# Kernel tuning notes

Measured on AMD Instinct MI355X. Metric: run time of the kernel, lower is better.

Reference implementation:

```python
import jax, jax.numpy as jnp
import numpy as np

NO, NR, E, D = 50000, 2000, 600000, 128
NEG_SLOPE = 0.2


def setup_inputs() -> dict:
    key = jax.random.key(0)
    ks = jax.random.split(key, 16)
    p = lambda k, shape: jax.random.normal(k, shape, dtype=jnp.float32) * 0.05
    return {
        "x_order": jax.random.normal(ks[0], (NO, D), dtype=jnp.float32),
        "x_rider": jax.random.normal(ks[1], (NR, D), dtype=jnp.float32),
        "order_idx": jax.random.randint(ks[2], (E,), 0, NO),
        "rider_idx": jax.random.randint(ks[3], (E,), 0, NR),
        # GATConv layer 1 (order_input_dim=128 -> hidden_dim=128, heads=1)
        "Ws1": p(ks[4], (D, D)), "Wd1": p(ks[5], (D, D)),
        "as1": p(ks[6], (D,)), "ad1": p(ks[7], (D,)), "b1": jnp.zeros((D,), jnp.float32),
        # GATConv layer 2 (hidden_dim=128 -> output_dim=128, heads=1)
        "Ws2": p(ks[8], (D, D)), "Wd2": p(ks[9], (D, D)),
        "as2": p(ks[10], (D,)), "ad2": p(ks[11], (D,)), "b2": jnp.zeros((D,), jnp.float32),
    }


def _segment_softmax(e, seg, num_segments):
    # numerically-stable softmax over edges grouped by destination node
    m = jax.ops.segment_max(e, seg, num_segments=num_segments)
    ex = jnp.exp(e - m[seg])
    s = jax.ops.segment_sum(ex, seg, num_segments=num_segments)
    return ex / (s[seg] + 1e-16)


def _gat_bipartite(x_src, x_dst, oi, ri, Ws, Wd, a_src, a_dst, b, n_dst):
    # PyG GATConv, heads=1, bipartite (src=order, dst=rider), no self-loops
    hs = x_src @ Ws            # [NO, D]
    hd = x_dst @ Wd            # [NR, D]
    alpha_s = hs @ a_src       # [NO]
    alpha_d = hd @ a_dst       # [NR]
    e = jax.nn.leaky_relu(alpha_s[oi] + alpha_d[ri], NEG_SLOPE)  # [E]
    alpha = _segment_softmax(e, ri, n_dst)                        # [E]
    out = jax.ops.segment_sum(alpha[:, None] * hs[oi], ri, num_segments=n_dst)
    return out + b


def reference(x_order, x_rider, order_idx, rider_idx,
              Ws1, Wd1, as1, ad1, b1, Ws2, Wd2, as2, ad2, b2):
    n_rider = x_rider.shape[0]
    # layer 1: update riders; order features pass through
    r1 = jax.nn.relu(_gat_bipartite(x_order, x_rider, order_idx, rider_idx,
                                    Ws1, Wd1, as1, ad1, b1, n_rider))
    o1 = jax.nn.relu(x_order)
    # layer 2
    r2 = _gat_bipartite(o1, r1, order_idx, rider_idx,
                        Ws2, Wd2, as2, ad2, b2, n_rider)
    # per-edge gather-dot-sigmoid scoring
    scores = jnp.sum(o1[order_idx] * r2[rider_idx], axis=1)
    return jax.nn.sigmoid(scores)
```

## Files before the change

### kernel.cpp

```cpp
#include <hip/hip_runtime.h>
#include <hip/hip_fp16.h>
#include <math.h>

#define NO 50000
#define NR 2000
#define NE 600000
#define D  128
#define NEG_SLOPE 0.2f
#define CAP 448
#define SLOT 512
#define NB 256
#define CH ((NE + NB - 1) / NB)

__global__ void precompute_wv(const float* __restrict__ Ws1, const float* __restrict__ as1,
                              const float* __restrict__ Wd1, const float* __restrict__ ad1,
                              const float* __restrict__ Ws2, const float* __restrict__ as2,
                              const float* __restrict__ Wd2, const float* __restrict__ ad2,
                              float* __restrict__ wsv1, float* __restrict__ wdv1,
                              float* __restrict__ wsv2, float* __restrict__ wdv2) {
    int k = threadIdx.x;
    float s1 = 0.f, d1 = 0.f, s2 = 0.f, d2 = 0.f;
    for (int j = 0; j < D; ++j) {
        s1 += Ws1[k * D + j] * as1[j];
        d1 += Wd1[k * D + j] * ad1[j];
        s2 += Ws2[k * D + j] * as2[j];
        d2 += Wd2[k * D + j] * ad2[j];
    }
    wsv1[k] = s1; wdv1[k] = d1; wsv2[k] = s2; wdv2[k] = d2;
}

__global__ void node_prep(const float* __restrict__ x, const float* __restrict__ xr,
                          const float* __restrict__ wsv1, const float* __restrict__ wsv2,
                          const float* __restrict__ wdv1,
                          float* __restrict__ as1o, float* __restrict__ as2o,
                          float* __restrict__ ad1r, __half* __restrict__ x16) {
    int lane = threadIdx.x & 63;
    if (blockIdx.x < NO / 4) {
        int row = blockIdx.x * 4 + (threadIdx.x >> 6);
        float2 xv = ((const float2*)(x + (size_t)row * D))[lane];
        float2 w1 = ((const float2*)wsv1)[lane];
        float2 w2 = ((const float2*)wsv2)[lane];
        float rx0 = fmaxf(xv.x, 0.f), rx1 = fmaxf(xv.y, 0.f);
        ((__half2*)(x16 + (size_t)row * D))[lane] = __floats2half2_rn(xv.x, xv.y);
        float a1 = xv.x * w1.x + xv.y * w1.y;
        float a2 = rx0 * w2.x + rx1 * w2.y;
        for (int off = 32; off; off >>= 1) {
            a1 += __shfl_down(a1, off);
            a2 += __shfl_down(a2, off);
        }
        if (lane == 0) { as1o[row] = a1; as2o[row] = a2; }
    } else {
        int row = (blockIdx.x - NO / 4) * 4 + (threadIdx.x >> 6);
        float2 xv = ((const float2*)(xr + (size_t)row * D))[lane];
        float2 w1 = ((const float2*)wdv1)[lane];
        float a = xv.x * w1.x + xv.y * w1.y;
        for (int off = 32; off; off >>= 1) a += __shfl_down(a, off);
        if (lane == 0) ad1r[row] = a;
    }
}


__global__ void blockhist_kernel(const int* __restrict__ ri, int* __restrict__ blockHist) {
    __shared__ int h[NR];
    int b = blockIdx.x, t = threadIdx.x;
    for (int i = t; i < NR; i += 256) h[i] = 0;
    __syncthreads();
    int lo = b * CH;
    int hi = lo + CH; if (hi > NE) hi = NE;
    for (int i = lo + t; i < hi; i += 256) atomicAdd(&h[ri[i]], 1);
    __syncthreads();
    for (int i = t; i < NR; i += 256) blockHist[(size_t)b * NR + i] = h[i];
}

__global__ void rowscan_kernel(int* __restrict__ blockHist, int* __restrict__ total) {
    int lane = threadIdx.x & 63;
    int r = blockIdx.x * 4 + (threadIdx.x >> 6);
    if (r >= NR) return;
    int b0 = lane * 4;
    int v0 = blockHist[(size_t)(b0 + 0) * NR + r];
    int v1 = blockHist[(size_t)(b0 + 1) * NR + r];
    int v2 = blockHist[(size_t)(b0 + 2) * NR + r];
    int v3 = blockHist[(size_t)(b0 + 3) * NR + r];
    int s = v0 + v1 + v2 + v3;
    int incl = s;
    for (int off = 1; off < 64; off <<= 1) {
        int u = __shfl_up(incl, off);
        if (lane >= off) incl += u;
    }
    int base = incl - s;
    blockHist[(size_t)(b0 + 0) * NR + r] = base;
    blockHist[(size_t)(b0 + 1) * NR + r] = base + v0;
    blockHist[(size_t)(b0 + 2) * NR + r] = base + v0 + v1;
    blockHist[(size_t)(b0 + 3) * NR + r] = base + v0 + v1 + v2;
    int tot = __shfl(incl, 63);
    if (lane == 0) total[r] = tot;
}

__global__ void scatter_kernel(const int* __restrict__ oi, const int* __restrict__ ri,
                               const int* __restrict__ blockHist,
                               int* __restrict__ sOrd, int* __restrict__ sEid) {
    __shared__ int h[NR];
    int b = blockIdx.x, t = threadIdx.x;
    for (int i = t; i < NR; i += 256) h[i] = 0;
    __syncthreads();
    int lo = b * CH;
    int hi = lo + CH; if (hi > NE) hi = NE;
    for (int i = lo + t; i < hi; i += 256) {
        int r = ri[i];
        int rank = atomicAdd(&h[r], 1);
        int pos = r * SLOT + blockHist[(size_t)b * NR + r] + rank;
        sOrd[pos] = oi[i];
        sEid[pos] = i;
    }
}

__global__ void __launch_bounds__(256)
rider_fused(const __half* __restrict__ x16,
            const float* __restrict__ as1o, const float* __restrict__ as2o,
            const float* __restrict__ ad1r,
            const int* __restrict__ cnt,
            const int* __restrict__ sOrd, const int* __restrict__ sEid,
            const float* __restrict__ W1, const float* __restrict__ b1,
            const float* __restrict__ wdv2,
            const float* __restrict__ W2, const float* __restrict__ b2,
            float* __restrict__ out) {
    __shared__ float eL[CAP];
    __shared__ float a2L[CAP];
    __shared__ int   sO[CAP];
    __shared__ int   sE[CAP];
    __shared__ float red[256];
    __shared__ float red8[256][9];
    __shared__ float tl[D];
    __shared__ float r2L[D];
    int r = blockIdx.x, t = threadIdx.x;
    int base = r * SLOT, n = cnt[r];
    float ad1 = ad1r[r];
    int grp = t >> 4, lh = t & 15;

    float s1 = 0.f;
    for (int i = t; i < n; i += 256) {
        int o = sOrd[base + i];
        float a2v = as2o[o];
        float e = as1o[o] + ad1;
        e = (e > 0.f) ? e : NEG_SLOPE * e;
        float ex = __expf(e);
        if (i < CAP) { eL[i] = ex; a2L[i] = a2v; sO[i] = o; sE[i] = sEid[base + i]; }
        s1 += ex;
    }
    red[t] = s1;
    __syncthreads();
    for (int off = 128; off; off >>= 1) {
        if (t < off) red[t] += red[t + off];
        __syncthreads();
    }
    float inv1 = 1.f / (red[0] + 1e-16f);
    __syncthreads();

    {
        float acc[8];
#pragma unroll
        for (int k = 0; k < 8; ++k) acc[k] = 0.f;
        if (n <= CAP) {
            int i = grp;
            for (; i + 16 < n; i += 32) {
                float a0 = eL[i], a1 = eL[i + 16];
                uint4 h0 = ((const uint4*)(x16 + (size_t)sO[i] * D))[lh];
                uint4 h1 = ((const uint4*)(x16 + (size_t)sO[i + 16] * D))[lh];
                const __half2* p0 = (const __half2*)&h0;
                const __half2* p1 = (const __half2*)&h1;
#pragma unroll
                for (int q = 0; q < 4; ++q) {
                    float2 f0 = __half22float2(p0[q]);
                    float2 f1 = __half22float2(p1[q]);
                    acc[2 * q]     += a0 * f0.x + a1 * f1.x;
                    acc[2 * q + 1] += a0 * f0.y + a1 * f1.y;
                }
            }
            if (i < n) {
                float a0 = eL[i];
                uint4 h0 = ((const uint4*)(x16 + (size_t)sO[i] * D))[lh];
                const __half2* p0 = (const __half2*)&h0;
#pragma unroll
                for (int q = 0; q < 4; ++q) {
                    float2 f0 = __half22float2(p0[q]);
                    acc[2 * q]     += a0 * f0.x;
                    acc[2 * q + 1] += a0 * f0.y;
                }
            }
        } else {
            for (int i = grp; i < n; i += 16) {
                float a0; int o;
                if (i < CAP) { a0 = eL[i]; o = sO[i]; }
                else {
                    o = sOrd[base + i];
                    float e = as1o[o] + ad1;
                    e = (e > 0.f) ? e : NEG_SLOPE * e;
                    a0 = __expf(e);
                }
                uint4 h0 = ((const uint4*)(x16 + (size_t)o * D))[lh];
                const __half2* p0 = (const __half2*)&h0;
#pragma unroll
                for (int q = 0; q < 4; ++q) {
                    float2 f0 = __half22float2(p0[q]);
                    acc[2 * q]     += a0 * f0.x;
                    acc[2 * q + 1] += a0 * f0.y;
                }
            }
        }
#pragma unroll
        for (int k = 0; k < 8; ++k) red8[t][k] = acc[k];
    }
    __syncthreads();
    if (t < D) {
        int lh2 = t >> 3, k = t & 7;
        float s = 0.f;
        for (int g = 0; g < 16; ++g) s += red8[g * 16 + lh2][k];
        tl[t] = s * inv1;
    }
    __syncthreads();

    {
        int d = t & 127, h = t >> 7;
        float a = 0.f;
        for (int k = h * 64; k < h * 64 + 64; ++k) a += tl[k] * W1[k * D + d];
        red[t] = a;
        __syncthreads();
        if (t < 128) red[t] = fmaxf(red[t] + red[t + 128] + b1[t], 0.f) * wdv2[t];
        __syncthreads();
        for (int off = 64; off; off >>= 1) {
            if (t < off) red[t] += red[t + off];
            __syncthreads();
        }
    }
    float ad2 = red[0];
    __syncthreads();

    float s2 = 0.f;
    for (int i = t; i < n; i += 256) {
        float a2v = (i < CAP) ? a2L[i] : as2o[sOrd[base + i]];
        float e = a2v + ad2;
        e = (e > 0.f) ? e : NEG_SLOPE * e;
        float ex = __expf(e);
        if (i < CAP) eL[i] = ex;
        s2 += ex;
    }
    red[t] = s2;
    __syncthreads();
    for (int off = 128; off; off >>= 1) {
        if (t < off) red[t] += red[t + off];
        __syncthreads();
    }
    float inv2 = 1.f / (red[0] + 1e-16f);
    __syncthreads();

    {
        float acc[8];
#pragma unroll
        for (int k = 0; k < 8; ++k) acc[k] = 0.f;
        if (n <= CAP) {
            int i = grp;
            for (; i + 16 < n; i += 32) {
                float a0 = eL[i], a1 = eL[i + 16];
                uint4 h0 = ((const uint4*)(x16 + (size_t)sO[i] * D))[lh];
                uint4 h1 = ((const uint4*)(x16 + (size_t)sO[i + 16] * D))[lh];
                const __half2* p0 = (const __half2*)&h0;
                const __half2* p1 = (const __half2*)&h1;
#pragma unroll
                for (int q = 0; q < 4; ++q) {
                    float2 f0 = __half22float2(p0[q]);
                    float2 f1 = __half22float2(p1[q]);
                    acc[2 * q]     += a0 * fmaxf(f0.x, 0.f) + a1 * fmaxf(f1.x, 0.f);
                    acc[2 * q + 1] += a0 * fmaxf(f0.y, 0.f) + a1 * fmaxf(f1.y, 0.f);
                }
            }
            if (i < n) {
                float a0 = eL[i];
                uint4 h0 = ((const uint4*)(x16 + (size_t)sO[i] * D))[lh];
                const __half2* p0 = (const __half2*)&h0;
#pragma unroll
                for (int q = 0; q < 4; ++q) {
                    float2 f0 = __half22float2(p0[q]);
                    acc[2 * q]     += a0 * fmaxf(f0.x, 0.f);
                    acc[2 * q + 1] += a0 * fmaxf(f0.y, 0.f);
                }
            }
        } else {
            for (int i = grp; i < n; i += 16) {
                float a0; int o;
                if (i < CAP) { a0 = eL[i]; o = sO[i]; }
                else {
                    o = sOrd[base + i];
                    float e = as2o[o] + ad2;
                    e = (e > 0.f) ? e : NEG_SLOPE * e;
                    a0 = __expf(e);
                }
                uint4 h0 = ((const uint4*)(x16 + (size_t)o * D))[lh];
                const __half2* p0 = (const __half2*)&h0;
#pragma unroll
                for (int q = 0; q < 4; ++q) {
                    float2 f0 = __half22float2(p0[q]);
                    acc[2 * q]     += a0 * fmaxf(f0.x, 0.f);
                    acc[2 * q + 1] += a0 * fmaxf(f0.y, 0.f);
                }
            }
        }
#pragma unroll
        for (int k = 0; k < 8; ++k) red8[t][k] = acc[k];
    }
    __syncthreads();
    if (t < D) {
        int lh2 = t >> 3, k = t & 7;
        float s = 0.f;
        for (int g = 0; g < 16; ++g) s += red8[g * 16 + lh2][k];
        tl[t] = s * inv2;
    }
    __syncthreads();

    {
        int d = t & 127, h = t >> 7;
        float a = 0.f;
        for (int k = h * 64; k < h * 64 + 64; ++k) a += tl[k] * W2[k * D + d];
        red[t] = a;
        __syncthreads();
        if (t < 128) r2L[t] = red[t] + red[t + 128] + b2[t];
        __syncthreads();
    }

    float rv[8];
#pragma unroll
    for (int k = 0; k < 8; ++k) rv[k] = r2L[lh * 8 + k];
    for (int i = grp; i < n; i += 16) {
        int o, eid;
        if (i < CAP) { o = sO[i]; eid = sE[i]; }
        else { o = sOrd[base + i]; eid = sEid[base + i]; }
        uint4 h0 = ((const uint4*)(x16 + (size_t)o * D))[lh];
        const __half2* p0 = (const __half2*)&h0;
        float p = 0.f;
#pragma unroll
        for (int q = 0; q < 4; ++q) {
            float2 f0 = __half22float2(p0[q]);
            p += fmaxf(f0.x, 0.f) * rv[2 * q] + fmaxf(f0.y, 0.f) * rv[2 * q + 1];
        }
        p += __shfl_xor(p, 8);
        p += __shfl_xor(p, 4);
        p += __shfl_xor(p, 2);
        p += __shfl_xor(p, 1);
        if (lh == 0) out[eid] = 1.f / (1.f + __expf(-p));
    }
}

extern "C" void kernel_launch(void* const* d_in, const int* in_sizes, int n_in,
                              void* d_out, int out_size, void* d_ws, size_t ws_size,
                              hipStream_t stream) {
    const float* x_order = (const float*)d_in[0];
    const float* x_rider = (const float*)d_in[1];
    const int*   oi      = (const int*)d_in[2];
    const int*   ri      = (const int*)d_in[3];
    const float* Ws1 = (const float*)d_in[4];
    const float* Wd1 = (const float*)d_in[5];
    const float* as1 = (const float*)d_in[6];
    const float* ad1 = (const float*)d_in[7];
    const float* b1  = (const float*)d_in[8];
    const float* Ws2 = (const float*)d_in[9];
    const float* Wd2 = (const float*)d_in[10];
    const float* as2 = (const float*)d_in[11];
    const float* ad2 = (const float*)d_in[12];
    const float* b2  = (const float*)d_in[13];
    float* out = (float*)d_out;

    char* w = (char*)d_ws;
    float* wsv1 = (float*)w; w += 512;
    float* wdv1 = (float*)w; w += 512;
    float* wsv2 = (float*)w; w += 512;
    float* wdv2 = (float*)w; w += 512;
    float* as1o = (float*)w; w += (size_t)NO * 4;
    float* as2o = (float*)w; w += (size_t)NO * 4;
    float* ad1r = (float*)w; w += (size_t)NR * 4;
    int* total  = (int*)w;   w += (size_t)NR * 4;
    int* blockHist = (int*)w; w += (size_t)NB * NR * 4;
    int* sOrd   = (int*)w;   w += (size_t)NR * SLOT * 4;
    int* sEid   = (int*)w;   w += (size_t)NR * SLOT * 4;
    __half* x16 = (__half*)w; w += (size_t)NO * D * 2;

    precompute_wv<<<1, 128, 0, stream>>>(Ws1, as1, Wd1, ad1, Ws2, as2, Wd2, ad2,
                                         wsv1, wdv1, wsv2, wdv2);
    node_prep<<<NO / 4 + NR / 4, 256, 0, stream>>>(x_order, x_rider, wsv1, wsv2, wdv1,
                                                   as1o, as2o, ad1r, x16);

    blockhist_kernel<<<NB, 256, 0, stream>>>(ri, blockHist);
    rowscan_kernel<<<NR / 4, 256, 0, stream>>>(blockHist, total);
    scatter_kernel<<<NB, 256, 0, stream>>>(oi, ri, blockHist, sOrd, sEid);

    rider_fused<<<NR, 256, 0, stream>>>(x16, as1o, as2o, ad1r, total, sOrd, sEid,
                                        Ws1, b1, wdv2, Ws2, b2, out);
}
```

Before: 246.9 us.

## Split fused rider kernel into layer-1 aggregation and layer-2 aggregate-score kernels

Splits the single per-rider fused kernel into two launches. The first does the layer-1 softmax aggregation and projection and writes the per-rider layer-2 attention scalar to a new workspace buffer. The second recomputes the neighbour list and exponentials, then does the layer-2 aggregation and edge scoring. Each kernel uses less shared memory and fewer registers, which may raise occupancy, and the layer-1 gather loop is unrolled four-wide for more loads in flight. The cost is an extra launch plus re-reading sOrd and the as2 values in the second kernel.

```diff
diff --git a/kernel.cpp b/kernel.cpp
--- a/kernel.cpp
+++ b/kernel.cpp
@@ -115,17 +115,142 @@
 }
 
 __global__ void __launch_bounds__(256)
-rider_fused(const __half* __restrict__ x16,
-            const float* __restrict__ as1o, const float* __restrict__ as2o,
-            const float* __restrict__ ad1r,
-            const int* __restrict__ cnt,
-            const int* __restrict__ sOrd, const int* __restrict__ sEid,
-            const float* __restrict__ W1, const float* __restrict__ b1,
-            const float* __restrict__ wdv2,
-            const float* __restrict__ W2, const float* __restrict__ b2,
-            float* __restrict__ out) {
+rider_agg1(const __half* __restrict__ x16, const float* __restrict__ as_o,
+           const float* __restrict__ ad_r,
+           const int* __restrict__ cnt, const int* __restrict__ sOrd,
+           const float* __restrict__ W, const float* __restrict__ bias,
+           const float* __restrict__ wdv2, float* __restrict__ ad2r) {
     __shared__ float eL[CAP];
-    __shared__ float a2L[CAP];
+    __shared__ int   sO[CAP];
+    __shared__ float red[256];
+    __shared__ float red8[256][9];
+    __shared__ float tl[D];
+    int r = blockIdx.x, t = threadIdx.x;
+    int base = r * SLOT, n = cnt[r];
+    float ad = ad_r[r];
+    int grp = t >> 4, lh = t & 15;
+
+    float ls = 0.f;
+    for (int i = t; i < n; i += 256) {
+        int o = sOrd[base + i];
+        float e = as_o[o] + ad;
+        e = (e > 0.f) ? e : NEG_SLOPE * e;
+        float ex = __expf(e);
+        if (i < CAP) { eL[i] = ex; sO[i] = o; }
+        ls += ex;
+    }
+    red[t] = ls;
+    __syncthreads();
+    for (int off = 128; off; off >>= 1) {
+        if (t < off) red[t] += red[t + off];
+        __syncthreads();
+    }
+    float inv = 1.f / (red[0] + 1e-16f);
+    __syncthreads();
+
+    float acc[8];
+#pragma unroll
+    for (int k = 0; k < 8; ++k) acc[k] = 0.f;
+    if (n <= CAP) {
+        int i = grp;
+        for (; i + 48 < n; i += 64) {
+            float a0 = eL[i], a1 = eL[i + 16], a2 = eL[i + 32], a3 = eL[i + 48];
+            uint4 h0 = ((const uint4*)(x16 + (size_t)sO[i]      * D))[lh];
+            uint4 h1 = ((const uint4*)(x16 + (size_t)sO[i + 16] * D))[lh];
+            uint4 h2 = ((const uint4*)(x16 + (size_t)sO[i + 32] * D))[lh];
+            uint4 h3 = ((const uint4*)(x16 + (size_t)sO[i + 48] * D))[lh];
+            const __half2* p0 = (const __half2*)&h0;
+            const __half2* p1 = (const __half2*)&h1;
+            const __half2* p2 = (const __half2*)&h2;
+            const __half2* p3 = (const __half2*)&h3;
+#pragma unroll
+            for (int q = 0; q < 4; ++q) {
+                float2 f0 = __half22float2(p0[q]);
+                float2 f1 = __half22float2(p1[q]);
+                float2 f2 = __half22float2(p2[q]);
+                float2 f3 = __half22float2(p3[q]);
+                acc[2 * q]     += a0 * f0.x + a1 * f1.x + a2 * f2.x + a3 * f3.x;
+                acc[2 * q + 1] += a0 * f0.y + a1 * f1.y + a2 * f2.y + a3 * f3.y;
+            }
+        }
+        for (; i + 16 < n; i += 32) {
+            float a0 = eL[i], a1 = eL[i + 16];
+            uint4 h0 = ((const uint4*)(x16 + (size_t)sO[i]      * D))[lh];
+            uint4 h1 = ((const uint4*)(x16 + (size_t)sO[i + 16] * D))[lh];
+            const __half2* p0 = (const __half2*)&h0;
+            const __half2* p1 = (const __half2*)&h1;
+#pragma unroll
+            for (int q = 0; q < 4; ++q) {
+                float2 f0 = __half22float2(p0[q]);
+                float2 f1 = __half22float2(p1[q]);
+                acc[2 * q]     += a0 * f0.x + a1 * f1.x;
+                acc[2 * q + 1] += a0 * f0.y + a1 * f1.y;
+            }
+        }
+        if (i < n) {
+            float a0 = eL[i];
+            uint4 h0 = ((const uint4*)(x16 + (size_t)sO[i] * D))[lh];
+            const __half2* p0 = (const __half2*)&h0;
+#pragma unroll
+            for (int q = 0; q < 4; ++q) {
+                float2 f0 = __half22float2(p0[q]);
+                acc[2 * q]     += a0 * f0.x;
+                acc[2 * q + 1] += a0 * f0.y;
+            }
+        }
+    } else {
+        for (int i = grp; i < n; i += 16) {
+            float a0; int o;
+            if (i < CAP) { a0 = eL[i]; o = sO[i]; }
+            else {
+                o = sOrd[base + i];
+                float e = as_o[o] + ad;
+                e = (e > 0.f) ? e : NEG_SLOPE * e;
+                a0 = __expf(e);
+            }
+            uint4 h0 = ((const uint4*)(x16 + (size_t)o * D))[lh];
+            const __half2* p0 = (const __half2*)&h0;
+#pragma unroll
+            for (int q = 0; q < 4; ++q) {
+                float2 f0 = __half22float2(p0[q]);
+                acc[2 * q]     += a0 * f0.x;
+                acc[2 * q + 1] += a0 * f0.y;
+            }
+        }
+    }
+#pragma unroll
+    for (int k = 0; k < 8; ++k) red8[t][k] = acc[k];
+    __syncthreads();
+    if (t < D) {
+        int lh2 = t >> 3, k = t & 7;
+        float s = 0.f;
+        for (int g = 0; g < 16; ++g) s += red8[g * 16 + lh2][k];
+        tl[t] = s * inv;
+    }
+    __syncthreads();
+
+    int d = t & 127, h = t >> 7;
+    float a2 = 0.f;
+    for (int k = h * 64; k < h * 64 + 64; ++k) a2 += tl[k] * W[k * D + d];
+    red[t] = a2;
+    __syncthreads();
+    if (t < 128) red[t] = fmaxf(red[t] + red[t + 128] + bias[t], 0.f) * wdv2[t];
+    __syncthreads();
+    for (int off = 64; off; off >>= 1) {
+        if (t < off) red[t] += red[t + off];
+        __syncthreads();
+    }
+    if (t == 0) ad2r[r] = red[0];
+}
+
+__global__ void __launch_bounds__(256)
+agg2_score(const __half* __restrict__ x16, const float* __restrict__ as_o,
+           const float* __restrict__ ad_r,
+           const int* __restrict__ cnt,
+           const int* __restrict__ sOrd, const int* __restrict__ sEid,
+           const float* __restrict__ W, const float* __restrict__ bias,
+           float* __restrict__ out) {
+    __shared__ float eL[CAP];
     __shared__ int   sO[CAP];
     __shared__ int   sE[CAP];
     __shared__ float red[256];
@@ -134,195 +259,95 @@
     __shared__ float r2L[D];
     int r = blockIdx.x, t = threadIdx.x;
     int base = r * SLOT, n = cnt[r];
-    float ad1 = ad1r[r];
+    float ad = ad_r[r];
     int grp = t >> 4, lh = t & 15;
 
-    float s1 = 0.f;
+    float ls = 0.f;
     for (int i = t; i < n; i += 256) {
         int o = sOrd[base + i];
-        float a2v = as2o[o];
-        float e = as1o[o] + ad1;
+        float e = as_o[o] + ad;
         e = (e > 0.f) ? e : NEG_SLOPE * e;
         float ex = __expf(e);
-        if (i < CAP) { eL[i] = ex; a2L[i] = a2v; sO[i] = o; sE[i] = sEid[base + i]; }
-        s1 += ex;
-    }
-    red[t] = s1;
+        if (i < CAP) { eL[i] = ex; sO[i] = o; sE[i] = sEid[base + i]; }
+        ls += ex;
+    }
+    red[t] = ls;
     __syncthreads();
     for (int off = 128; off; off >>= 1) {
         if (t < off) red[t] += red[t + off];
         __syncthreads();
     }
-    float inv1 = 1.f / (red[0] + 1e-16f);
-    __syncthreads();
-
-    {
-        float acc[8];
-#pragma unroll
-        for (int k = 0; k < 8; ++k) acc[k] = 0.f;
-        if (n <= CAP) {
-            int i = grp;
-            for (; i + 16 < n; i += 32) {
-                float a0 = eL[i], a1 = eL[i + 16];
-                uint4 h0 = ((const uint4*)(x16 + (size_t)sO[i] * D))[lh];
-                uint4 h1 = ((const uint4*)(x16 + (size_t)sO[i + 16] * D))[lh];
-                const __half2* p0 = (const __half2*)&h0;
-                const __half2* p1 = (const __half2*)&h1;
-#pragma unroll
-                for (int q = 0; q < 4; ++q) {
-                    float2 f0 = __half22float2(p0[q]);
-                    float2 f1 = __half22float2(p1[q]);
-                    acc[2 * q]     += a0 * f0.x + a1 * f1.x;
-                    acc[2 * q + 1] += a0 * f0.y + a1 * f1.y;
-                }
-            }
-            if (i < n) {
-                float a0 = eL[i];
-                uint4 h0 = ((const uint4*)(x16 + (size_t)sO[i] * D))[lh];
-                const __half2* p0 = (const __half2*)&h0;
-#pragma unroll
-                for (int q = 0; q < 4; ++q) {
-                    float2 f0 = __half22float2(p0[q]);
-                    acc[2 * q]     += a0 * f0.x;
-                    acc[2 * q + 1] += a0 * f0.y;
-                }
-            }
-        } else {
-            for (int i = grp; i < n; i += 16) {
-                float a0; int o;
-                if (i < CAP) { a0 = eL[i]; o = sO[i]; }
-                else {
-                    o = sOrd[base + i];
-                    float e = as1o[o] + ad1;
-                    e = (e > 0.f) ? e : NEG_SLOPE * e;
-                    a0 = __expf(e);
-                }
-                uint4 h0 = ((const uint4*)(x16 + (size_t)o * D))[lh];
-                const __half2* p0 = (const __half2*)&h0;
-#pragma unroll
-                for (int q = 0; q < 4; ++q) {
-                    float2 f0 = __half22float2(p0[q]);
-                    acc[2 * q]     += a0 * f0.x;
-                    acc[2 * q + 1] += a0 * f0.y;
-                }
-            }
-        }
-#pragma unroll
-        for (int k = 0; k < 8; ++k) red8[t][k] = acc[k];
-    }
+    float inv = 1.f / (red[0] + 1e-16f);
+    __syncthreads();
+
+    float acc[8];
+#pragma unroll
+    for (int k = 0; k < 8; ++k) acc[k] = 0.f;
+    if (n <= CAP) {
+        int i = grp;
+        for (; i + 16 < n; i += 32) {
+            float a0 = eL[i], a1 = eL[i + 16];
+            uint4 h0 = ((const uint4*)(x16 + (size_t)sO[i]      * D))[lh];
+            uint4 h1 = ((const uint4*)(x16 + (size_t)sO[i + 16] * D))[lh];
+            const __half2* p0 = (const __half2*)&h0;
+            const __half2* p1 = (const __half2*)&h1;
+#pragma unroll
+            for (int q = 0; q < 4; ++q) {
+                float2 f0 = __half22float2(p0[q]);
+                float2 f1 = __half22float2(p1[q]);
+                acc[2 * q]     += a0 * fmaxf(f0.x, 0.f) + a1 * fmaxf(f1.x, 0.f);
+                acc[2 * q + 1] += a0 * fmaxf(f0.y, 0.f) + a1 * fmaxf(f1.y, 0.f);
+            }
+        }
+        if (i < n) {
+            float a0 = eL[i];
+            uint4 h0 = ((const uint4*)(x16 + (size_t)sO[i] * D))[lh];
+            const __half2* p0 = (const __half2*)&h0;
+#pragma unroll
+            for (int q = 0; q < 4; ++q) {
+                float2 f0 = __half22float2(p0[q]);
+                acc[2 * q]     += a0 * fmaxf(f0.x, 0.f);
+                acc[2 * q + 1] += a0 * fmaxf(f0.y, 0.f);
+            }
+        }
+    } else {
+        for (int i = grp; i < n; i += 16) {
+            float a0; int o;
+            if (i < CAP) { a0 = eL[i]; o = sO[i]; }
+            else {
+                o = sOrd[base + i];
+                float e = as_o[o] + ad;
+                e = (e > 0.f) ? e : NEG_SLOPE * e;
+                a0 = __expf(e);
+            }
+            uint4 h0 = ((const uint4*)(x16 + (size_t)o * D))[lh];
+            const __half2* p0 = (const __half2*)&h0;
+#pragma unroll
+            for (int q = 0; q < 4; ++q) {
+                float2 f0 = __half22float2(p0[q]);
+                acc[2 * q]     += a0 * fmaxf(f0.x, 0.f);
+                acc[2 * q + 1] += a0 * fmaxf(f0.y, 0.f);
+            }
+        }
+    }
+#pragma unroll
+    for (int k = 0; k < 8; ++k) red8[t][k] = acc[k];
     __syncthreads();
     if (t < D) {
         int lh2 = t >> 3, k = t & 7;
         float s = 0.f;
         for (int g = 0; g < 16; ++g) s += red8[g * 16 + lh2][k];
-        tl[t] = s * inv1;
+        tl[t] = s * inv;
     }
     __syncthreads();
 
     {
         int d = t & 127, h = t >> 7;
         float a = 0.f;
-        for (int k = h * 64; k < h * 64 + 64; ++k) a += tl[k] * W1[k * D + d];
+        for (int k = h * 64; k < h * 64 + 64; ++k) a += tl[k] * W[k * D + d];
         red[t] = a;
         __syncthreads();
-        if (t < 128) red[t] = fmaxf(red[t] + red[t + 128] + b1[t], 0.f) * wdv2[t];
-        __syncthreads();
-        for (int off = 64; off; off >>= 1) {
-            if (t < off) red[t] += red[t + off];
-            __syncthreads();
-        }
-    }
-    float ad2 = red[0];
-    __syncthreads();
-
-    float s2 = 0.f;
-    for (int i = t; i < n; i += 256) {
-        float a2v = (i < CAP) ? a2L[i] : as2o[sOrd[base + i]];
-        float e = a2v + ad2;
-        e = (e > 0.f) ? e : NEG_SLOPE * e;
-        float ex = __expf(e);
-        if (i < CAP) eL[i] = ex;
-        s2 += ex;
-    }
-    red[t] = s2;
-    __syncthreads();
-    for (int off = 128; off; off >>= 1) {
-        if (t < off) red[t] += red[t + off];
-        __syncthreads();
-    }
-    float inv2 = 1.f / (red[0] + 1e-16f);
-    __syncthreads();
-
-    {
-        float acc[8];
-#pragma unroll
-        for (int k = 0; k < 8; ++k) acc[k] = 0.f;
-        if (n <= CAP) {
-            int i = grp;
-            for (; i + 16 < n; i += 32) {
-                float a0 = eL[i], a1 = eL[i + 16];
-                uint4 h0 = ((const uint4*)(x16 + (size_t)sO[i] * D))[lh];
-                uint4 h1 = ((const uint4*)(x16 + (size_t)sO[i + 16] * D))[lh];
-                const __half2* p0 = (const __half2*)&h0;
-                const __half2* p1 = (const __half2*)&h1;
-#pragma unroll
-                for (int q = 0; q < 4; ++q) {
-                    float2 f0 = __half22float2(p0[q]);
-                    float2 f1 = __half22float2(p1[q]);
-                    acc[2 * q]     += a0 * fmaxf(f0.x, 0.f) + a1 * fmaxf(f1.x, 0.f);
-                    acc[2 * q + 1] += a0 * fmaxf(f0.y, 0.f) + a1 * fmaxf(f1.y, 0.f);
-                }
-            }
-            if (i < n) {
-                float a0 = eL[i];
-                uint4 h0 = ((const uint4*)(x16 + (size_t)sO[i] * D))[lh];
-                const __half2* p0 = (const __half2*)&h0;
-#pragma unroll
-                for (int q = 0; q < 4; ++q) {
-                    float2 f0 = __half22float2(p0[q]);
-                    acc[2 * q]     += a0 * fmaxf(f0.x, 0.f);
-                    acc[2 * q + 1] += a0 * fmaxf(f0.y, 0.f);
-                }
-            }
-        } else {
-            for (int i = grp; i < n; i += 16) {
-                float a0; int o;
-                if (i < CAP) { a0 = eL[i]; o = sO[i]; }
-                else {
-                    o = sOrd[base + i];
-                    float e = as2o[o] + ad2;
-                    e = (e > 0.f) ? e : NEG_SLOPE * e;
-                    a0 = __expf(e);
-                }
-                uint4 h0 = ((const uint4*)(x16 + (size_t)o * D))[lh];
-                const __half2* p0 = (const __half2*)&h0;
-#pragma unroll
-                for (int q = 0; q < 4; ++q) {
-                    float2 f0 = __half22float2(p0[q]);
-                    acc[2 * q]     += a0 * fmaxf(f0.x, 0.f);
-                    acc[2 * q + 1] += a0 * fmaxf(f0.y, 0.f);
-                }
-            }
-        }
-#pragma unroll
-        for (int k = 0; k < 8; ++k) red8[t][k] = acc[k];
-    }
-    __syncthreads();
-    if (t < D) {
-        int lh2 = t >> 3, k = t & 7;
-        float s = 0.f;
-        for (int g = 0; g < 16; ++g) s += red8[g * 16 + lh2][k];
-        tl[t] = s * inv2;
-    }
-    __syncthreads();
-
-    {
-        int d = t & 127, h = t >> 7;
-        float a = 0.f;
-        for (int k = h * 64; k < h * 64 + 64; ++k) a += tl[k] * W2[k * D + d];
-        red[t] = a;
-        __syncthreads();
-        if (t < 128) r2L[t] = red[t] + red[t + 128] + b2[t];
+        if (t < 128) r2L[t] = red[t] + red[t + 128] + bias[t];
         __syncthreads();
     }
 
@@ -376,6 +401,7 @@
     float* as1o = (float*)w; w += (size_t)NO * 4;
     float* as2o = (float*)w; w += (size_t)NO * 4;
     float* ad1r = (float*)w; w += (size_t)NR * 4;
+    float* ad2r = (float*)w; w += (size_t)NR * 4;
     int* total  = (int*)w;   w += (size_t)NR * 4;
     int* blockHist = (int*)w; w += (size_t)NB * NR * 4;
     int* sOrd   = (int*)w;   w += (size_t)NR * SLOT * 4;
@@ -391,6 +417,8 @@
     rowscan_kernel<<<NR / 4, 256, 0, stream>>>(blockHist, total);
     scatter_kernel<<<NB, 256, 0, stream>>>(oi, ri, blockHist, sOrd, sEid);
 
-    rider_fused<<<NR, 256, 0, stream>>>(x16, as1o, as2o, ad1r, total, sOrd, sEid,
-                                        Ws1, b1, wdv2, Ws2, b2, out);
-}
+    rider_agg1<<<NR, 256, 0, stream>>>(x16, as1o, ad1r, total, sOrd,
+                                       Ws1, b1, wdv2, ad2r);
+    agg2_score<<<NR, 256, 0, stream>>>(x16, as2o, ad2r, total, sOrd, sEid,
+                                       Ws2, b2, out);
+}
```

New measurement: 243.8 us. About the same (-1.3%).

## Merge prep kernels and move edge scoring into a separate edge-parallel kernel

Applied to the files above, without the earlier changes.

Merges the weight-vector precompute into the histogram kernel and the row scan into the node-prep kernel, cutting two launches. Edge scoring now runs in a new kernel parallel over edges in the original edge order, reading per-rider r2 stored as fp16, so the sEid scatter array and its writes go away. The work of each 2000-block rider kernel is shortened. The cost is an extra launch and a global round-trip for r2, plus reduced precision from storing r2 in fp16.

```diff
diff --git a/kernel.cpp b/kernel.cpp
--- a/kernel.cpp
+++ b/kernel.cpp
@@ -12,31 +12,47 @@
 #define NB 256
 #define CH ((NE + NB - 1) / NB)
 
-__global__ void precompute_wv(const float* __restrict__ Ws1, const float* __restrict__ as1,
-                              const float* __restrict__ Wd1, const float* __restrict__ ad1,
-                              const float* __restrict__ Ws2, const float* __restrict__ as2,
-                              const float* __restrict__ Wd2, const float* __restrict__ ad2,
-                              float* __restrict__ wsv1, float* __restrict__ wdv1,
-                              float* __restrict__ wsv2, float* __restrict__ wdv2) {
-    int k = threadIdx.x;
-    float s1 = 0.f, d1 = 0.f, s2 = 0.f, d2 = 0.f;
-    for (int j = 0; j < D; ++j) {
-        s1 += Ws1[k * D + j] * as1[j];
-        d1 += Wd1[k * D + j] * ad1[j];
-        s2 += Ws2[k * D + j] * as2[j];
-        d2 += Wd2[k * D + j] * ad2[j];
-    }
-    wsv1[k] = s1; wdv1[k] = d1; wsv2[k] = s2; wdv2[k] = d2;
-}
-
-__global__ void node_prep(const float* __restrict__ x, const float* __restrict__ xr,
+__global__ void prep_hist(const int* __restrict__ ri, int* __restrict__ blockHist,
+                          const float* __restrict__ Ws1, const float* __restrict__ as1,
+                          const float* __restrict__ Wd1, const float* __restrict__ ad1,
+                          const float* __restrict__ Ws2, const float* __restrict__ as2,
+                          const float* __restrict__ Wd2, const float* __restrict__ ad2,
+                          float* __restrict__ wsv1, float* __restrict__ wdv1,
+                          float* __restrict__ wsv2, float* __restrict__ wdv2) {
+    __shared__ int h[NR];
+    int t = threadIdx.x;
+    if (blockIdx.x < NB) {
+        int b = blockIdx.x;
+        for (int i = t; i < NR; i += 256) h[i] = 0;
+        __syncthreads();
+        int lo = b * CH;
+        int hi = lo + CH; if (hi > NE) hi = NE;
+        for (int i = lo + t; i < hi; i += 256) atomicAdd(&h[ri[i]], 1);
+        __syncthreads();
+        for (int i = t; i < NR; i += 256) blockHist[(size_t)b * NR + i] = h[i];
+    } else if (t < 128) {
+        int k = t;
+        float s1 = 0.f, d1 = 0.f, s2 = 0.f, d2 = 0.f;
+        for (int j = 0; j < D; ++j) {
+            s1 += Ws1[k * D + j] * as1[j];
+            d1 += Wd1[k * D + j] * ad1[j];
+            s2 += Ws2[k * D + j] * as2[j];
+            d2 += Wd2[k * D + j] * ad2[j];
+        }
+        wsv1[k] = s1; wdv1[k] = d1; wsv2[k] = s2; wdv2[k] = d2;
+    }
+}
+
+__global__ void prep_scan(const float* __restrict__ x, const float* __restrict__ xr,
                           const float* __restrict__ wsv1, const float* __restrict__ wsv2,
                           const float* __restrict__ wdv1,
                           float* __restrict__ as1o, float* __restrict__ as2o,
-                          float* __restrict__ ad1r, __half* __restrict__ x16) {
+                          float* __restrict__ ad1r, __half* __restrict__ x16,
+                          int* __restrict__ blockHist, int* __restrict__ total) {
     int lane = threadIdx.x & 63;
-    if (blockIdx.x < NO / 4) {
-        int row = blockIdx.x * 4 + (threadIdx.x >> 6);
+    int b = blockIdx.x;
+    if (b < NO / 4) {
+        int row = b * 4 + (threadIdx.x >> 6);
         float2 xv = ((const float2*)(x + (size_t)row * D))[lane];
         float2 w1 = ((const float2*)wsv1)[lane];
         float2 w2 = ((const float2*)wsv2)[lane];
@@ -49,56 +65,41 @@
             a2 += __shfl_down(a2, off);
         }
         if (lane == 0) { as1o[row] = a1; as2o[row] = a2; }
-    } else {
-        int row = (blockIdx.x - NO / 4) * 4 + (threadIdx.x >> 6);
+    } else if (b < NO / 4 + NR / 4) {
+        int row = (b - NO / 4) * 4 + (threadIdx.x >> 6);
         float2 xv = ((const float2*)(xr + (size_t)row * D))[lane];
         float2 w1 = ((const float2*)wdv1)[lane];
         float a = xv.x * w1.x + xv.y * w1.y;
         for (int off = 32; off; off >>= 1) a += __shfl_down(a, off);
         if (lane == 0) ad1r[row] = a;
-    }
-}
-
-
-__global__ void blockhist_kernel(const int* __restrict__ ri, int* __restrict__ blockHist) {
-    __shared__ int h[NR];
-    int b = blockIdx.x, t = threadIdx.x;
-    for (int i = t; i < NR; i += 256) h[i] = 0;
-    __syncthreads();
-    int lo = b * CH;
-    int hi = lo + CH; if (hi > NE) hi = NE;
-    for (int i = lo + t; i < hi; i += 256) atomicAdd(&h[ri[i]], 1);
-    __syncthreads();
-    for (int i = t; i < NR; i += 256) blockHist[(size_t)b * NR + i] = h[i];
-}
-
-__global__ void rowscan_kernel(int* __restrict__ blockHist, int* __restrict__ total) {
-    int lane = threadIdx.x & 63;
-    int r = blockIdx.x * 4 + (threadIdx.x >> 6);
-    if (r >= NR) return;
-    int b0 = lane * 4;
-    int v0 = blockHist[(size_t)(b0 + 0) * NR + r];
-    int v1 = blockHist[(size_t)(b0 + 1) * NR + r];
-    int v2 = blockHist[(size_t)(b0 + 2) * NR + r];
-    int v3 = blockHist[(size_t)(b0 + 3) * NR + r];
-    int s = v0 + v1 + v2 + v3;
-    int incl = s;
-    for (int off = 1; off < 64; off <<= 1) {
-        int u = __shfl_up(incl, off);
-        if (lane >= off) incl += u;
-    }
-    int base = incl - s;
-    blockHist[(size_t)(b0 + 0) * NR + r] = base;
-    blockHist[(size_t)(b0 + 1) * NR + r] = base + v0;
-    blockHist[(size_t)(b0 + 2) * NR + r] = base + v0 + v1;
-    blockHist[(size_t)(b0 + 3) * NR + r] = base + v0 + v1 + v2;
-    int tot = __shfl(incl, 63);
-    if (lane == 0) total[r] = tot;
+    } else {
+        int v = b - (NO / 4 + NR / 4);
+        int r = v * 4 + (threadIdx.x >> 6);
+        if (r >= NR) return;
+        int b0 = lane * 4;
+        int v0 = blockHist[(size_t)(b0 + 0) * NR + r];
+        int v1 = blockHist[(size_t)(b0 + 1) * NR + r];
+        int v2 = blockHist[(size_t)(b0 + 2) * NR + r];
+        int v3 = blockHist[(size_t)(b0 + 3) * NR + r];
+        int s = v0 + v1 + v2 + v3;
+        int incl = s;
+        for (int off = 1; off < 64; off <<= 1) {
+            int u = __shfl_up(incl, off);
+            if (lane >= off) incl += u;
+        }
+        int base = incl - s;
+        blockHist[(size_t)(b0 + 0) * NR + r] = base;
+        blockHist[(size_t)(b0 + 1) * NR + r] = base + v0;
+        blockHist[(size_t)(b0 + 2) * NR + r] = base + v0 + v1;
+        blockHist[(size_t)(b0 + 3) * NR + r] = base + v0 + v1 + v2;
+        int tot = __shfl(incl, 63);
+        if (lane == 0) total[r] = tot;
+    }
 }
 
 __global__ void scatter_kernel(const int* __restrict__ oi, const int* __restrict__ ri,
                                const int* __restrict__ blockHist,
-                               int* __restrict__ sOrd, int* __restrict__ sEid) {
+                               int* __restrict__ sOrd) {
     __shared__ int h[NR];
     int b = blockIdx.x, t = threadIdx.x;
     for (int i = t; i < NR; i += 256) h[i] = 0;
@@ -110,44 +111,38 @@
         int rank = atomicAdd(&h[r], 1);
         int pos = r * SLOT + blockHist[(size_t)b * NR + r] + rank;
         sOrd[pos] = oi[i];
-        sEid[pos] = i;
     }
 }
 
 __global__ void __launch_bounds__(256)
-rider_fused(const __half* __restrict__ x16,
-            const float* __restrict__ as1o, const float* __restrict__ as2o,
-            const float* __restrict__ ad1r,
-            const int* __restrict__ cnt,
-            const int* __restrict__ sOrd, const int* __restrict__ sEid,
-            const float* __restrict__ W1, const float* __restrict__ b1,
-            const float* __restrict__ wdv2,
-            const float* __restrict__ W2, const float* __restrict__ b2,
-            float* __restrict__ out) {
+agg12(const __half* __restrict__ x16,
+      const float* __restrict__ as1o, const float* __restrict__ as2o,
+      const float* __restrict__ ad1r,
+      const int* __restrict__ cnt, const int* __restrict__ sOrd,
+      const float* __restrict__ W1, const float* __restrict__ b1,
+      const float* __restrict__ wdv2,
+      const float* __restrict__ W2, const float* __restrict__ b2,
+      __half* __restrict__ r216) {
     __shared__ float eL[CAP];
-    __shared__ float a2L[CAP];
     __shared__ int   sO[CAP];
-    __shared__ int   sE[CAP];
     __shared__ float red[256];
     __shared__ float red8[256][9];
     __shared__ float tl[D];
-    __shared__ float r2L[D];
     int r = blockIdx.x, t = threadIdx.x;
     int base = r * SLOT, n = cnt[r];
+    int grp = t >> 4, lh = t & 15;
+
     float ad1 = ad1r[r];
-    int grp = t >> 4, lh = t & 15;
-
-    float s1 = 0.f;
+    float ls = 0.f;
     for (int i = t; i < n; i += 256) {
         int o = sOrd[base + i];
-        float a2v = as2o[o];
         float e = as1o[o] + ad1;
         e = (e > 0.f) ? e : NEG_SLOPE * e;
         float ex = __expf(e);
-        if (i < CAP) { eL[i] = ex; a2L[i] = a2v; sO[i] = o; sE[i] = sEid[base + i]; }
-        s1 += ex;
-    }
-    red[t] = s1;
+        if (i < CAP) { eL[i] = ex; sO[i] = o; }
+        ls += ex;
+    }
+    red[t] = ls;
     __syncthreads();
     for (int off = 128; off; off >>= 1) {
         if (t < off) red[t] += red[t + off];
@@ -164,7 +159,7 @@
             int i = grp;
             for (; i + 16 < n; i += 32) {
                 float a0 = eL[i], a1 = eL[i + 16];
-                uint4 h0 = ((const uint4*)(x16 + (size_t)sO[i] * D))[lh];
+                uint4 h0 = ((const uint4*)(x16 + (size_t)sO[i]      * D))[lh];
                 uint4 h1 = ((const uint4*)(x16 + (size_t)sO[i + 16] * D))[lh];
                 const __half2* p0 = (const __half2*)&h0;
                 const __half2* p1 = (const __half2*)&h1;
@@ -235,16 +230,16 @@
     float ad2 = red[0];
     __syncthreads();
 
-    float s2 = 0.f;
+    float ls2 = 0.f;
     for (int i = t; i < n; i += 256) {
-        float a2v = (i < CAP) ? a2L[i] : as2o[sOrd[base + i]];
-        float e = a2v + ad2;
+        int o = (i < CAP) ? sO[i] : sOrd[base + i];
+        float e = as2o[o] + ad2;
         e = (e > 0.f) ? e : NEG_SLOPE * e;
         float ex = __expf(e);
         if (i < CAP) eL[i] = ex;
-        s2 += ex;
-    }
-    red[t] = s2;
+        ls2 += ex;
+    }
+    red[t] = ls2;
     __syncthreads();
     for (int off = 128; off; off >>= 1) {
         if (t < off) red[t] += red[t + off];
@@ -261,7 +256,7 @@
             int i = grp;
             for (; i + 16 < n; i += 32) {
                 float a0 = eL[i], a1 = eL[i + 16];
-                uint4 h0 = ((const uint4*)(x16 + (size_t)sO[i] * D))[lh];
+                uint4 h0 = ((const uint4*)(x16 + (size_t)sO[i]      * D))[lh];
                 uint4 h1 = ((const uint4*)(x16 + (size_t)sO[i + 16] * D))[lh];
                 const __half2* p0 = (const __half2*)&h0;
                 const __half2* p1 = (const __half2*)&h1;
@@ -322,31 +317,37 @@
         for (int k = h * 64; k < h * 64 + 64; ++k) a += tl[k] * W2[k * D + d];
         red[t] = a;
         __syncthreads();
-        if (t < 128) r2L[t] = red[t] + red[t + 128] + b2[t];
-        __syncthreads();
-    }
-
-    float rv[8];
-#pragma unroll
-    for (int k = 0; k < 8; ++k) rv[k] = r2L[lh * 8 + k];
-    for (int i = grp; i < n; i += 16) {
-        int o, eid;
-        if (i < CAP) { o = sO[i]; eid = sE[i]; }
-        else { o = sOrd[base + i]; eid = sEid[base + i]; }
-        uint4 h0 = ((const uint4*)(x16 + (size_t)o * D))[lh];
-        const __half2* p0 = (const __half2*)&h0;
-        float p = 0.f;
-#pragma unroll
-        for (int q = 0; q < 4; ++q) {
-            float2 f0 = __half22float2(p0[q]);
-            p += fmaxf(f0.x, 0.f) * rv[2 * q] + fmaxf(f0.y, 0.f) * rv[2 * q + 1];
-        }
-        p += __shfl_xor(p, 8);
-        p += __shfl_xor(p, 4);
-        p += __shfl_xor(p, 2);
-        p += __shfl_xor(p, 1);
-        if (lh == 0) out[eid] = 1.f / (1.f + __expf(-p));
-    }
+        if (t < 128) r216[(size_t)r * D + t] = __float2half(red[t] + red[t + 128] + b2[t]);
+    }
+}
+
+__global__ void score_edges(const __half* __restrict__ x16, const __half* __restrict__ r216,
+                            const int* __restrict__ oi, const int* __restrict__ ri,
+                            float* __restrict__ out) {
+    int gid = blockIdx.x * blockDim.x + threadIdx.x;
+    int e  = gid >> 4;
+    int lh = gid & 15;
+    if (e >= NE) return;
+    int o = oi[e], r = ri[e];
+    uint4 hx = ((const uint4*)(x16  + (size_t)o * D))[lh];
+    uint4 hr = ((const uint4*)(r216 + (size_t)r * D))[lh];
+    float2 a0 = __half22float2(*(const __half2*)&hx.x);
+    float2 a1 = __half22float2(*(const __half2*)&hx.y);
+    float2 a2 = __half22float2(*(const __half2*)&hx.z);
+    float2 a3 = __half22float2(*(const __half2*)&hx.w);
+    float2 b0 = __half22float2(*(const __half2*)&hr.x);
+    float2 b1 = __half22float2(*(const __half2*)&hr.y);
+    float2 b2 = __half22float2(*(const __half2*)&hr.z);
+    float2 b3 = __half22float2(*(const __half2*)&hr.w);
+    float p = fmaxf(a0.x, 0.f) * b0.x + fmaxf(a0.y, 0.f) * b0.y +
+              fmaxf(a1.x, 0.f) * b1.x + fmaxf(a1.y, 0.f) * b1.y +
+              fmaxf(a2.x, 0.f) * b2.x + fmaxf(a2.y, 0.f) * b2.y +
+              fmaxf(a3.x, 0.f) * b3.x + fmaxf(a3.y, 0.f) * b3.y;
+    p += __shfl_xor(p, 8);
+    p += __shfl_xor(p, 4);
+    p += __shfl_xor(p, 2);
+    p += __shfl_xor(p, 1);
+    if (lh == 0) out[e] = 1.f / (1.f + __expf(-p));
 }
 
 extern "C" void kernel_launch(void* const* d_in, const int* in_sizes, int n_in,
@@ -379,18 +380,18 @@
     int* total  = (int*)w;   w += (size_t)NR * 4;
     int* blockHist = (int*)w; w += (size_t)NB * NR * 4;
     int* sOrd   = (int*)w;   w += (size_t)NR * SLOT * 4;
-    int* sEid   = (int*)w;   w += (size_t)NR * SLOT * 4;
-    __half* x16 = (__half*)w; w += (size_t)NO * D * 2;
-
-    precompute_wv<<<1, 128, 0, stream>>>(Ws1, as1, Wd1, ad1, Ws2, as2, Wd2, ad2,
-                                         wsv1, wdv1, wsv2, wdv2);
-    node_prep<<<NO / 4 + NR / 4, 256, 0, stream>>>(x_order, x_rider, wsv1, wsv2, wdv1,
-                                                   as1o, as2o, ad1r, x16);
-
-    blockhist_kernel<<<NB, 256, 0, stream>>>(ri, blockHist);
-    rowscan_kernel<<<NR / 4, 256, 0, stream>>>(blockHist, total);
-    scatter_kernel<<<NB, 256, 0, stream>>>(oi, ri, blockHist, sOrd, sEid);
-
-    rider_fused<<<NR, 256, 0, stream>>>(x16, as1o, as2o, ad1r, total, sOrd, sEid,
-                                        Ws1, b1, wdv2, Ws2, b2, out);
-}
+    __half* x16  = (__half*)w; w += (size_t)NO * D * 2;
+    __half* r216 = (__half*)w; w += (size_t)NR * D * 2;
+
+    prep_hist<<<NB + 1, 256, 0, stream>>>(ri, blockHist,
+                                          Ws1, as1, Wd1, ad1, Ws2, as2, Wd2, ad2,
+                                          wsv1, wdv1, wsv2, wdv2);
+    prep_scan<<<NO / 4 + NR / 4 + 500, 256, 0, stream>>>(x_order, x_rider,
+                                                         wsv1, wsv2, wdv1,
+                                                         as1o, as2o, ad1r, x16,
+                                                         blockHist, total);
+    scatter_kernel<<<NB, 256, 0, stream>>>(oi, ri, blockHist, sOrd);
+    agg12<<<NR, 256, 0, stream>>>(x16, as1o, as2o, ad1r, total, sOrd,
+                                  Ws1, b1, wdv2, Ws2, b2, r216);
+    score_edges<<<(NE * 16 + 255) / 256, 256, 0, stream>>>(x16, r216, oi, ri, out);
+}
```

Measured after the change: 221.7 us, median of 2. -10.2%, faster.
